# Kernel optimization log

Measured on AMD Instinct MI355X. Metric: run time of the kernel, lower is better.

Reference implementation:

```python
import jax, jax.numpy as jnp
import numpy as np

N_NODES = 100000
N_EDGES = 1280000
D_IN = 64
D_HID = 128
D_OUT = 64


def sage_conv(x, src, dst, W_l, b_l, W_r, n_nodes):
    # PyG SAGEConv (aggr='mean', root_weight=True):
    #   out_i = W_l @ mean_{j in N(i)} x_j + b_l + W_r @ x_i
    msg = x[src]  # [E, d] gather of source-node features
    agg = jax.ops.segment_sum(msg, dst, num_segments=n_nodes)  # [N, d]
    cnt = jax.ops.segment_sum(jnp.ones((src.shape[0], 1), x.dtype), dst,
                              num_segments=n_nodes)  # [N, 1]
    mean = agg / jnp.maximum(cnt, 1.0)  # zero-neighbor nodes -> 0 (matches scatter-mean)
    return mean @ W_l.T + b_l + x @ W_r.T


def setup_inputs() -> dict:
    key = jax.random.key(0)
    ks = jax.random.split(key, 8)
    x = jax.random.normal(ks[0], (N_NODES, D_IN), dtype=jnp.float32)
    edge_index = jax.random.randint(ks[1], (2, N_EDGES), 0, N_NODES, dtype=jnp.int64)
    s = 0.05
    W_l1 = jax.random.normal(ks[2], (D_HID, D_IN), dtype=jnp.float32) * s
    b_l1 = jnp.zeros((D_HID,), dtype=jnp.float32)
    W_r1 = jax.random.normal(ks[3], (D_HID, D_IN), dtype=jnp.float32) * s
    W_l2 = jax.random.normal(ks[4], (D_OUT, D_HID), dtype=jnp.float32) * s
    b_l2 = jnp.zeros((D_OUT,), dtype=jnp.float32)
    W_r2 = jax.random.normal(ks[5], (D_OUT, D_HID), dtype=jnp.float32) * s
    return {"x": x, "edge_index": edge_index,
            "W_l1": W_l1, "b_l1": b_l1, "W_r1": W_r1,
            "W_l2": W_l2, "b_l2": b_l2, "W_r2": W_r2}


def reference(x, edge_index, W_l1, b_l1, W_r1, W_l2, b_l2, W_r2):
    src, dst = edge_index[0], edge_index[1]
    n = x.shape[0]
    h = sage_conv(x, src, dst, W_l1, b_l1, W_r1, n)
    h = jax.nn.relu(h)
    out = sage_conv(h, src, dst, W_l2, b_l2, W_r2, n)
    return out
```

## Files before the change

### kernel.cpp

```cpp
#include <hip/hip_runtime.h>
#include <cstdint>
#include <cstddef>

typedef __attribute__((ext_vector_type(8))) short short8;
typedef __attribute__((ext_vector_type(4))) float floatx4;
typedef __attribute__((ext_vector_type(2))) float floatx2;
typedef __attribute__((ext_vector_type(4))) int intx4;

static constexpr int DIN  = 64;
static constexpr int DHID = 128;
static constexpr int BSH  = 7;
static constexpr int BNODES = 1 << BSH;
static constexpr int TILE = 8192;
static constexpr int CAP  = 4096;
static constexpr unsigned SENT = 0xFFFFFFFFu;

__device__ inline short f2bf(float f) {
  unsigned u = __float_as_uint(f);
  u += 0x7FFF + ((u >> 16) & 1);
  return (short)(u >> 16);
}
__device__ inline float bf2f(short s) {
  return __uint_as_float(((unsigned)(unsigned short)s) << 16);
}
__device__ inline floatx2 bfpair(unsigned u) {
  floatx2 r;
  r[0] = __uint_as_float(u << 16);
  r[1] = __uint_as_float(u & 0xFFFF0000u);
  return r;
}

__global__ __launch_bounds__(256) void part_prep_kernel(const void* edges, long long nmax,
    int* __restrict__ bucket_cursor, int* __restrict__ real_cnt,
    unsigned* __restrict__ packed, int E, int NB,
    const float* __restrict__ x,
    const float* __restrict__ Wl1, const float* __restrict__ Wr1,
    const float* __restrict__ Wl2, const float* __restrict__ Wr2,
    short* __restrict__ xb, short* __restrict__ wc1, short* __restrict__ wc2,
    int nx, int gP, int gx)
{
  __shared__ unsigned sval[TILE];
  __shared__ unsigned saux[TILE];
  __shared__ int hist[1024];
  __shared__ int gb[1024];
  __shared__ int smode;
  int t = threadIdx.x;
  int blk = blockIdx.x;
  if (blk >= gP) {
    int b = blk - gP;
    if (b < gx) {
      int i0 = (b * 256 + t) * 8;
      if (i0 < nx) {
        floatx4 f0 = *(const floatx4*)&x[i0];
        floatx4 f1 = *(const floatx4*)&x[i0 + 4];
        short8 o;
        o[0]=f2bf(f0[0]); o[1]=f2bf(f0[1]); o[2]=f2bf(f0[2]); o[3]=f2bf(f0[3]);
        o[4]=f2bf(f1[0]); o[5]=f2bf(f1[1]); o[6]=f2bf(f1[2]); o[7]=f2bf(f1[3]);
        *(short8*)&xb[i0] = o;
      }
    } else {
      int wb = b - gx;
      int idx = ((wb & 15) * 256 + t) * 4;
      int n = idx >> 7, k = idx & 127;
      const float* src;
      if (wb < 16) src = (k < 64) ? &Wl1[n * 64 + k] : &Wr1[n * 64 + (k - 64)];
      else         src = (n < 64) ? &Wl2[n * 128 + k] : &Wr2[(n - 64) * 128 + k];
      floatx4 f = *(const floatx4*)src;
      short* dst = (wb < 16 ? wc1 : wc2) + idx;
      dst[0]=f2bf(f[0]); dst[1]=f2bf(f[1]); dst[2]=f2bf(f[2]); dst[3]=f2bf(f[3]);
    }
    return;
  }
  int base = blk * TILE;
  int cnt_here = E - base; if (cnt_here > TILE) cnt_here = TILE;
  for (int i = t; i < NB; i += 256) hist[i] = 0;
  if (t == 0) smode = 1;
  __syncthreads();
  {
    const long long* e64 = (const long long*)edges;
    int nchk = E < 256 ? E : 256;
    bool ok = true;
    for (int i = t; i < nchk; i += 256) {
      long long v = e64[i];
      if (v < 0 || v >= nmax) ok = false;
    }
    if (!ok) smode = 0;
  }
  __syncthreads();
  bool m64 = (smode != 0);
  #pragma unroll 4
  for (int c = 0; c < TILE / 256; ++c) {
    int idx = c * 256 + t;
    if (idx < cnt_here) {
      int i = base + idx;
      int s, d;
      if (m64) { const long long* e = (const long long*)edges; s = (int)e[i]; d = (int)e[(size_t)E + i]; }
      else     { const int*       e = (const int*)edges;       s = e[i];      d = e[(size_t)E + i]; }
      int b = d >> BSH;
      int rank = atomicAdd(&hist[b], 1);
      sval[idx] = ((unsigned)(d & (BNODES - 1)) << 17) | (unsigned)s;
      saux[idx] = ((unsigned)b << 13) | (unsigned)rank;
    }
  }
  __syncthreads();
  for (int b = t; b < NB; b += 256) {
    int cnt = hist[b];
    int gbase = 0;
    if (cnt > 0) {
      int pad = (cnt + 15) & ~15;
      gbase = b * CAP + atomicAdd(&bucket_cursor[b], pad);
      atomicAdd(&real_cnt[b], cnt);
      for (int j = cnt; j < pad; ++j) packed[gbase + j] = SENT;
    }
    gb[b] = gbase;
  }
  __syncthreads();
  #pragma unroll 4
  for (int c = 0; c < TILE / 256; ++c) {
    int idx = c * 256 + t;
    if (idx < cnt_here) {
      unsigned a = saux[idx];
      packed[gb[a >> 13] + (a & 0x1FFFu)] = sval[idx];
    }
  }
}

__global__ __launch_bounds__(256) void bucket_sort_kernel(const unsigned* __restrict__ packed,
                                                          const int* __restrict__ bucket_cursor,
                                                          const int* __restrict__ real_cnt,
                                                          int* __restrict__ row_ptr,
                                                          int* __restrict__ sorted_src, int N, int E) {
  __shared__ int nhist[BNODES];
  __shared__ int cur[BNODES];
  __shared__ int wsum[4];
  __shared__ int redsum[4];
  int b = blockIdx.x, t = threadIdx.x;
  int partial = 0;
  for (int i = t; i < b; i += 256) partial += real_cnt[i];
  #pragma unroll
  for (int off = 1; off < 64; off <<= 1) partial += __shfl_xor(partial, off, 64);
  if ((t & 63) == 0) redsum[t >> 6] = partial;
  if (t < BNODES) nhist[t] = 0;
  if (b == 0 && t == 0) row_ptr[N] = E;
  __syncthreads();
  int eb = redsum[0] + redsum[1] + redsum[2] + redsum[3];
  int n0 = b << BSH;
  int nn = N - n0; if (nn > BNODES) nn = BNODES;
  int rbeg = b * CAP, rcnt = bucket_cursor[b];
  for (int i = t; i < rcnt; i += 256) {
    unsigned p = packed[rbeg + i];
    if (p != SENT) atomicAdd(&nhist[p >> 17], 1);
  }
  __syncthreads();
  int lane = t & 63, w = t >> 6;
  int v = (t < BNODES) ? nhist[t] : 0;
  int val = v;
  #pragma unroll
  for (int off = 1; off < 64; off <<= 1) {
    int u = __shfl_up(val, off, 64);
    if (lane >= off) val += u;
  }
  if (lane == 63) wsum[w] = val;
  __syncthreads();
  int pre = (w == 1) ? wsum[0] : 0;
  int excl = pre + val - v;
  if (t < nn) { row_ptr[n0 + t] = eb + excl; cur[t] = eb + excl; }
  __syncthreads();
  for (int i = t; i < rcnt; i += 256) {
    unsigned p = packed[rbeg + i];
    if (p != SENT) {
      int pos = atomicAdd(&cur[p >> 17], 1);
      sorted_src[pos] = (int)(p & 0x1FFFFu);
    }
  }
}

template <bool EPI>
__global__ __launch_bounds__(256) void agg_bf16_kernel(const short* __restrict__ feat,
                                                       const int* __restrict__ row_ptr,
                                                       const int* __restrict__ srcs,
                                                       const float* __restrict__ rbuf,
                                                       const float* __restrict__ bias,
                                                       short* __restrict__ outb,
                                                       float* __restrict__ outf, int N) {
  int node = blockIdx.x * 32 + (threadIdx.x >> 3);
  if (node >= N) return;
  int c = threadIdx.x & 7;
  const short* fbase = feat + c * 8;
  int beg = row_ptr[node], end = row_ptr[node + 1];
  floatx2 acc2[4];
  #pragma unroll
  for (int k = 0; k < 4; ++k) acc2[k] = (floatx2){0.f, 0.f};
  int e = beg;
  for (; e + 8 <= end; e += 8) {
    intx4 sa = *(const intx4*)&srcs[e];
    intx4 sb = *(const intx4*)&srcs[e + 4];
    short8 v0 = *(const short8*)&fbase[(size_t)sa[0] * 64];
    short8 v1 = *(const short8*)&fbase[(size_t)sa[1] * 64];
    short8 v2 = *(const short8*)&fbase[(size_t)sa[2] * 64];
    short8 v3 = *(const short8*)&fbase[(size_t)sa[3] * 64];
    short8 v4 = *(const short8*)&fbase[(size_t)sb[0] * 64];
    short8 v5 = *(const short8*)&fbase[(size_t)sb[1] * 64];
    short8 v6 = *(const short8*)&fbase[(size_t)sb[2] * 64];
    short8 v7 = *(const short8*)&fbase[(size_t)sb[3] * 64];
    const unsigned* u0 = (const unsigned*)&v0;
    const unsigned* u1 = (const unsigned*)&v1;
    const unsigned* u2 = (const unsigned*)&v2;
    const unsigned* u3 = (const unsigned*)&v3;
    const unsigned* u4 = (const unsigned*)&v4;
    const unsigned* u5 = (const unsigned*)&v5;
    const unsigned* u6 = (const unsigned*)&v6;
    const unsigned* u7 = (const unsigned*)&v7;
    #pragma unroll
    for (int k = 0; k < 4; ++k) {
      floatx2 s01 = bfpair(u0[k]) + bfpair(u1[k]);
      floatx2 s23 = bfpair(u2[k]) + bfpair(u3[k]);
      floatx2 s45 = bfpair(u4[k]) + bfpair(u5[k]);
      floatx2 s67 = bfpair(u6[k]) + bfpair(u7[k]);
      acc2[k] += (s01 + s23) + (s45 + s67);
    }
  }
  for (; e + 4 <= end; e += 4) {
    intx4 sa = *(const intx4*)&srcs[e];
    short8 v0 = *(const short8*)&fbase[(size_t)sa[0] * 64];
    short8 v1 = *(const short8*)&fbase[(size_t)sa[1] * 64];
    short8 v2 = *(const short8*)&fbase[(size_t)sa[2] * 64];
    short8 v3 = *(const short8*)&fbase[(size_t)sa[3] * 64];
    const unsigned* u0 = (const unsigned*)&v0;
    const unsigned* u1 = (const unsigned*)&v1;
    const unsigned* u2 = (const unsigned*)&v2;
    const unsigned* u3 = (const unsigned*)&v3;
    #pragma unroll
    for (int k = 0; k < 4; ++k) {
      floatx2 s01 = bfpair(u0[k]) + bfpair(u1[k]);
      floatx2 s23 = bfpair(u2[k]) + bfpair(u3[k]);
      acc2[k] += s01 + s23;
    }
  }
  for (; e < end; ++e) {
    short8 v = *(const short8*)&fbase[(size_t)srcs[e] * 64];
    const unsigned* u = (const unsigned*)&v;
    #pragma unroll
    for (int k = 0; k < 4; ++k) acc2[k] += bfpair(u[k]);
  }
  float acc[8];
  #pragma unroll
  for (int k = 0; k < 4; ++k) { acc[2 * k] = acc2[k][0]; acc[2 * k + 1] = acc2[k][1]; }
  float inv = 1.f / fmaxf((float)(end - beg), 1.f);
  if (!EPI) {
    short8 o;
    #pragma unroll
    for (int j = 0; j < 8; ++j) o[j] = f2bf(acc[j] * inv);
    *(short8*)&outb[(size_t)node * 64 + c * 8] = o;
  } else {
    floatx4 b0 = *(const floatx4*)&bias[c * 8];
    floatx4 b1 = *(const floatx4*)&bias[c * 8 + 4];
    floatx4 r0 = *(const floatx4*)&rbuf[(size_t)node * 64 + c * 8];
    floatx4 r1 = *(const floatx4*)&rbuf[(size_t)node * 64 + c * 8 + 4];
    floatx4 o0, o1;
    #pragma unroll
    for (int j = 0; j < 4; ++j) {
      o0[j] = acc[j] * inv + b0[j] + r0[j];
      o1[j] = acc[4 + j] * inv + b1[j] + r1[j];
    }
    *(floatx4*)&outf[(size_t)node * 64 + c * 8]     = o0;
    *(floatx4*)&outf[(size_t)node * 64 + c * 8 + 4] = o1;
  }
}

__global__ __launch_bounds__(256) void fused_gemm_kernel(
    const short* __restrict__ Aa, const short* __restrict__ Ab,
    const short* __restrict__ wc1, const short* __restrict__ wc2,
    const float* __restrict__ bias1,
    short* __restrict__ Cg, float* __restrict__ Cr, int M)
{
  __shared__ short Ws[128][136];
  __shared__ short Hs[64][136];
  int t = threadIdx.x;
  #pragma unroll
  for (int i = 0; i < 8; ++i) {
    int idx = i * 256 + t;
    int r = idx >> 4, c8 = (idx & 15) * 8;
    *(short8*)&Ws[r][c8] = *(const short8*)&wc1[r * 128 + c8];
  }
  __syncthreads();
  int wv = t >> 6, lane = t & 63, q = lane >> 4, l15 = lane & 15;
  int m0 = blockIdx.x * 64 + wv * 16;
  int row = m0 + l15;
  bool rowok = row < M;
  floatx4 acc[8];
  #pragma unroll
  for (int nt = 0; nt < 8; ++nt) acc[nt] = (floatx4){0.f, 0.f, 0.f, 0.f};
  #pragma unroll
  for (int ko = 0; ko < 4; ++ko) {
    const short* Asrc = (ko < 2) ? Aa : Ab;
    short8 a = {0, 0, 0, 0, 0, 0, 0, 0};
    if (rowok) a = *(const short8*)&Asrc[(size_t)row * 64 + (ko & 1) * 32 + q * 8];
    #pragma unroll
    for (int nt = 0; nt < 8; ++nt) {
      short8 b = *(const short8*)&Ws[nt * 16 + l15][ko * 32 + q * 8];
      acc[nt] = __builtin_amdgcn_mfma_f32_16x16x32_bf16(a, b, acc[nt], 0, 0, 0);
    }
  }
  #pragma unroll
  for (int nt = 0; nt < 8; ++nt) {
    int n = nt * 16 + l15;
    float bv = bias1[n];
    #pragma unroll
    for (int r2 = 0; r2 < 4; ++r2) {
      int lr = wv * 16 + q * 4 + r2;
      float v = fmaxf(acc[nt][r2] + bv, 0.f);
      Hs[lr][n] = f2bf(v);
    }
  }
  __syncthreads();
  #pragma unroll
  for (int i = 0; i < 8; ++i) {
    int idx = i * 256 + t;
    int r = idx >> 4, c8 = (idx & 15) * 8;
    *(short8*)&Ws[r][c8] = *(const short8*)&wc2[r * 128 + c8];
  }
  __syncthreads();
  #pragma unroll
  for (int nt = 0; nt < 8; ++nt) acc[nt] = (floatx4){0.f, 0.f, 0.f, 0.f};
  #pragma unroll
  for (int ko = 0; ko < 4; ++ko) {
    short8 a = *(const short8*)&Hs[wv * 16 + l15][ko * 32 + q * 8];
    #pragma unroll
    for (int nt = 0; nt < 8; ++nt) {
      short8 b = *(const short8*)&Ws[nt * 16 + l15][ko * 32 + q * 8];
      acc[nt] = __builtin_amdgcn_mfma_f32_16x16x32_bf16(a, b, acc[nt], 0, 0, 0);
    }
  }
  #pragma unroll
  for (int nt = 0; nt < 8; ++nt) {
    int n = nt * 16 + l15;
    #pragma unroll
    for (int r2 = 0; r2 < 4; ++r2) {
      int mr = m0 + q * 4 + r2;
      if (mr >= M) continue;
      float v = acc[nt][r2];
      if (nt < 4) Cg[(size_t)mr * 64 + n] = f2bf(v);
      else        Cr[(size_t)mr * 64 + (n - 64)] = v;
    }
  }
}

extern "C" void kernel_launch(void* const* d_in, const int* in_sizes, int n_in,
                              void* d_out, int out_size, void* d_ws, size_t ws_size,
                              hipStream_t stream) {
  const float* x   = (const float*)d_in[0];
  const void*  ei  = d_in[1];
  const float* Wl1 = (const float*)d_in[2];
  const float* bl1 = (const float*)d_in[3];
  const float* Wr1 = (const float*)d_in[4];
  const float* Wl2 = (const float*)d_in[5];
  const float* bl2 = (const float*)d_in[6];
  const float* Wr2 = (const float*)d_in[7];
  int N = in_sizes[0] / DIN;
  int E = in_sizes[1] / 2;
  int NB = (N + BNODES - 1) / BNODES;

  char* w = (char*)d_ws;
  size_t off = 0;
  auto alloc = [&](size_t bytes) -> void* {
    void* p = w + off;
    off += (bytes + 255) & ~(size_t)255;
    return p;
  };
  int*      bcur       = (int*)alloc((size_t)NB * 8);
  int*      rcnt       = bcur + NB;
  int*      row_ptr    = (int*)alloc(((size_t)N + 1) * 4);
  unsigned* packed     = (unsigned*)alloc((size_t)NB * CAP * 4);
  int*      sorted_src = (int*)alloc((size_t)E * 4);
  short*    xb         = (short*)alloc((size_t)N * 64 * 2);
  short*    meanb      = (short*)alloc((size_t)N * 64 * 2);
  float*    rbuf       = (float*)alloc((size_t)N * 64 * 4);
  short*    wc1        = (short*)alloc(128 * 128 * 2);
  short*    wc2        = (short*)alloc(128 * 128 * 2);
  (void)ws_size; (void)n_in; (void)out_size;

  hipMemsetAsync(bcur, 0, (size_t)NB * 8, stream);

  int nx = N * DIN;
  int gx = (nx / 8 + 255) / 256;
  int gP = (E + TILE - 1) / TILE;
  part_prep_kernel<<<gP + gx + 32, 256, 0, stream>>>(ei, (long long)N, bcur, rcnt, packed,
                                                     E, NB, x, Wl1, Wr1, Wl2, Wr2,
                                                     xb, wc1, wc2, nx, gP, gx);

  bucket_sort_kernel<<<NB, 256, 0, stream>>>(packed, bcur, rcnt, row_ptr, sorted_src, N, E);

  int gN32 = (N + 31) / 32;
  agg_bf16_kernel<false><<<gN32, 256, 0, stream>>>(xb, row_ptr, sorted_src, nullptr, nullptr, meanb, nullptr, N);

  int gm = (N + 63) / 64;
  fused_gemm_kernel<<<gm, 256, 0, stream>>>(meanb, xb, wc1, wc2, bl1, meanb, rbuf, N);

  agg_bf16_kernel<true><<<gN32, 256, 0, stream>>>(meanb, row_ptr, sorted_src, rbuf, bl2, nullptr, (float*)d_out, N);
}
```

Before: 203.5 us.

## Fuse first-layer mean aggregation into bucket sort and double GEMM row tile

The bucket sort kernel now keeps each bucket's sorted edge list in shared memory and computes the first-layer neighbor mean for its 128 nodes right away. This removes one kernel launch and the global re-read of row_ptr and sorted_src for the first aggregation. The fused GEMM now handles 128 rows per block, with two MFMA row tiles per wave sharing each B fragment, so fewer weight tiles are loaded into shared memory. In exchange, the sort kernel uses more LDS (a 16KB edge list) and only 128 nodes per block do the gather, which may reduce occupancy and parallelism during aggregation.

After: 201.1 us. No clear change (-1.2%).

```diff
diff --git a/kernel.cpp b/kernel.cpp
--- a/kernel.cpp
+++ b/kernel.cpp
@@ -125,13 +125,14 @@
   }
 }
 
-__global__ __launch_bounds__(256) void bucket_sort_kernel(const unsigned* __restrict__ packed,
-                                                          const int* __restrict__ bucket_cursor,
-                                                          const int* __restrict__ real_cnt,
-                                                          int* __restrict__ row_ptr,
-                                                          int* __restrict__ sorted_src, int N, int E) {
+__global__ __launch_bounds__(256) void bucket_sort_agg_kernel(const unsigned* __restrict__ packed,
+    const int* __restrict__ bucket_cursor, const int* __restrict__ real_cnt,
+    int* __restrict__ row_ptr, int* __restrict__ sorted_src,
+    const short* __restrict__ feat, short* __restrict__ meanb, int N, int E) {
   __shared__ int nhist[BNODES];
   __shared__ int cur[BNODES];
+  __shared__ int begs[BNODES];
+  __shared__ int elist[CAP];
   __shared__ int wsum[4];
   __shared__ int redsum[4];
   int b = blockIdx.x, t = threadIdx.x;
@@ -164,25 +165,81 @@
   __syncthreads();
   int pre = (w == 1) ? wsum[0] : 0;
   int excl = pre + val - v;
-  if (t < nn) { row_ptr[n0 + t] = eb + excl; cur[t] = eb + excl; }
+  if (t < nn) { row_ptr[n0 + t] = eb + excl; cur[t] = excl; begs[t] = excl; }
   __syncthreads();
   for (int i = t; i < rcnt; i += 256) {
     unsigned p = packed[rbeg + i];
     if (p != SENT) {
       int pos = atomicAdd(&cur[p >> 17], 1);
-      sorted_src[pos] = (int)(p & 0x1FFFFu);
-    }
-  }
-}
-
-template <bool EPI>
-__global__ __launch_bounds__(256) void agg_bf16_kernel(const short* __restrict__ feat,
-                                                       const int* __restrict__ row_ptr,
-                                                       const int* __restrict__ srcs,
-                                                       const float* __restrict__ rbuf,
-                                                       const float* __restrict__ bias,
-                                                       short* __restrict__ outb,
-                                                       float* __restrict__ outf, int N) {
+      int s = (int)(p & 0x1FFFFu);
+      elist[pos] = s;
+      sorted_src[eb + pos] = s;
+    }
+  }
+  __syncthreads();
+  int c = t & 7;
+  const short* fbase = feat + c * 8;
+  #pragma unroll
+  for (int ch = 0; ch < 4; ++ch) {
+    int ln = ch * 32 + (t >> 3);
+    if (ln < nn) {
+      int beg = begs[ln], end = cur[ln];
+      floatx2 acc2[4];
+      #pragma unroll
+      for (int k = 0; k < 4; ++k) acc2[k] = (floatx2){0.f, 0.f};
+      int e = beg;
+      for (; e + 8 <= end; e += 8) {
+        int s0 = elist[e],     s1 = elist[e + 1], s2 = elist[e + 2], s3 = elist[e + 3];
+        int s4 = elist[e + 4], s5 = elist[e + 5], s6 = elist[e + 6], s7 = elist[e + 7];
+        short8 v0 = *(const short8*)&fbase[(size_t)s0 * 64];
+        short8 v1 = *(const short8*)&fbase[(size_t)s1 * 64];
+        short8 v2 = *(const short8*)&fbase[(size_t)s2 * 64];
+        short8 v3 = *(const short8*)&fbase[(size_t)s3 * 64];
+        short8 v4 = *(const short8*)&fbase[(size_t)s4 * 64];
+        short8 v5 = *(const short8*)&fbase[(size_t)s5 * 64];
+        short8 v6 = *(const short8*)&fbase[(size_t)s6 * 64];
+        short8 v7 = *(const short8*)&fbase[(size_t)s7 * 64];
+        const unsigned* u0 = (const unsigned*)&v0;
+        const unsigned* u1 = (const unsigned*)&v1;
+        const unsigned* u2 = (const unsigned*)&v2;
+        const unsigned* u3 = (const unsigned*)&v3;
+        const unsigned* u4 = (const unsigned*)&v4;
+        const unsigned* u5 = (const unsigned*)&v5;
+        const unsigned* u6 = (const unsigned*)&v6;
+        const unsigned* u7 = (const unsigned*)&v7;
+        #pragma unroll
+        for (int k = 0; k < 4; ++k) {
+          floatx2 s01 = bfpair(u0[k]) + bfpair(u1[k]);
+          floatx2 s23 = bfpair(u2[k]) + bfpair(u3[k]);
+          floatx2 s45 = bfpair(u4[k]) + bfpair(u5[k]);
+          floatx2 s67 = bfpair(u6[k]) + bfpair(u7[k]);
+          acc2[k] += (s01 + s23) + (s45 + s67);
+        }
+      }
+      for (; e < end; ++e) {
+        short8 vv = *(const short8*)&fbase[(size_t)elist[e] * 64];
+        const unsigned* uu = (const unsigned*)&vv;
+        #pragma unroll
+        for (int k = 0; k < 4; ++k) acc2[k] += bfpair(uu[k]);
+      }
+      float inv = 1.f / fmaxf((float)(end - beg), 1.f);
+      short8 o;
+      #pragma unroll
+      for (int k = 0; k < 4; ++k) {
+        o[2 * k]     = f2bf(acc2[k][0] * inv);
+        o[2 * k + 1] = f2bf(acc2[k][1] * inv);
+      }
+      *(short8*)&meanb[(size_t)(n0 + ln) * 64 + c * 8] = o;
+    }
+  }
+}
+
+__global__ __launch_bounds__(256) void agg_epi_kernel(const short* __restrict__ feat,
+                                                      const int* __restrict__ row_ptr,
+                                                      const int* __restrict__ srcs,
+                                                      const float* __restrict__ rbuf,
+                                                      const float* __restrict__ bias,
+                                                      float* __restrict__ outf, int N) {
   int node = blockIdx.x * 32 + (threadIdx.x >> 3);
   if (node >= N) return;
   int c = threadIdx.x & 7;
@@ -247,25 +304,18 @@
   #pragma unroll
   for (int k = 0; k < 4; ++k) { acc[2 * k] = acc2[k][0]; acc[2 * k + 1] = acc2[k][1]; }
   float inv = 1.f / fmaxf((float)(end - beg), 1.f);
-  if (!EPI) {
-    short8 o;
-    #pragma unroll
-    for (int j = 0; j < 8; ++j) o[j] = f2bf(acc[j] * inv);
-    *(short8*)&outb[(size_t)node * 64 + c * 8] = o;
-  } else {
-    floatx4 b0 = *(const floatx4*)&bias[c * 8];
-    floatx4 b1 = *(const floatx4*)&bias[c * 8 + 4];
-    floatx4 r0 = *(const floatx4*)&rbuf[(size_t)node * 64 + c * 8];
-    floatx4 r1 = *(const floatx4*)&rbuf[(size_t)node * 64 + c * 8 + 4];
-    floatx4 o0, o1;
-    #pragma unroll
-    for (int j = 0; j < 4; ++j) {
-      o0[j] = acc[j] * inv + b0[j] + r0[j];
-      o1[j] = acc[4 + j] * inv + b1[j] + r1[j];
-    }
-    *(floatx4*)&outf[(size_t)node * 64 + c * 8]     = o0;
-    *(floatx4*)&outf[(size_t)node * 64 + c * 8 + 4] = o1;
-  }
+  floatx4 b0 = *(const floatx4*)&bias[c * 8];
+  floatx4 b1 = *(const floatx4*)&bias[c * 8 + 4];
+  floatx4 r0 = *(const floatx4*)&rbuf[(size_t)node * 64 + c * 8];
+  floatx4 r1 = *(const floatx4*)&rbuf[(size_t)node * 64 + c * 8 + 4];
+  floatx4 o0, o1;
+  #pragma unroll
+  for (int j = 0; j < 4; ++j) {
+    o0[j] = acc[j] * inv + b0[j] + r0[j];
+    o1[j] = acc[4 + j] * inv + b1[j] + r1[j];
+  }
+  *(floatx4*)&outf[(size_t)node * 64 + c * 8]     = o0;
+  *(floatx4*)&outf[(size_t)node * 64 + c * 8 + 4] = o1;
 }
 
 __global__ __launch_bounds__(256) void fused_gemm_kernel(
@@ -275,7 +325,7 @@
     short* __restrict__ Cg, float* __restrict__ Cr, int M)
 {
   __shared__ short Ws[128][136];
-  __shared__ short Hs[64][136];
+  __shared__ short Hs[128][136];
   int t = threadIdx.x;
   #pragma unroll
   for (int i = 0; i < 8; ++i) {
@@ -285,32 +335,41 @@
   }
   __syncthreads();
   int wv = t >> 6, lane = t & 63, q = lane >> 4, l15 = lane & 15;
-  int m0 = blockIdx.x * 64 + wv * 16;
-  int row = m0 + l15;
-  bool rowok = row < M;
-  floatx4 acc[8];
-  #pragma unroll
-  for (int nt = 0; nt < 8; ++nt) acc[nt] = (floatx4){0.f, 0.f, 0.f, 0.f};
+  int m0 = blockIdx.x * 128 + wv * 32;
+  floatx4 acc[2][8];
+  #pragma unroll
+  for (int mt = 0; mt < 2; ++mt)
+    #pragma unroll
+    for (int nt = 0; nt < 8; ++nt) acc[mt][nt] = (floatx4){0.f, 0.f, 0.f, 0.f};
   #pragma unroll
   for (int ko = 0; ko < 4; ++ko) {
     const short* Asrc = (ko < 2) ? Aa : Ab;
-    short8 a = {0, 0, 0, 0, 0, 0, 0, 0};
-    if (rowok) a = *(const short8*)&Asrc[(size_t)row * 64 + (ko & 1) * 32 + q * 8];
+    short8 a[2];
+    #pragma unroll
+    for (int mt = 0; mt < 2; ++mt) {
+      int row = m0 + mt * 16 + l15;
+      a[mt] = (short8){0, 0, 0, 0, 0, 0, 0, 0};
+      if (row < M) a[mt] = *(const short8*)&Asrc[(size_t)row * 64 + (ko & 1) * 32 + q * 8];
+    }
     #pragma unroll
     for (int nt = 0; nt < 8; ++nt) {
-      short8 b = *(const short8*)&Ws[nt * 16 + l15][ko * 32 + q * 8];
-      acc[nt] = __builtin_amdgcn_mfma_f32_16x16x32_bf16(a, b, acc[nt], 0, 0, 0);
-    }
-  }
-  #pragma unroll
-  for (int nt = 0; nt < 8; ++nt) {
-    int n = nt * 16 + l15;
-    float bv = bias1[n];
-    #pragma unroll
-    for (int r2 = 0; r2 < 4; ++r2) {
-      int lr = wv * 16 + q * 4 + r2;
-      float v = fmaxf(acc[nt][r2] + bv, 0.f);
-      Hs[lr][n] = f2bf(v);
+      short8 bfr = *(const short8*)&Ws[nt * 16 + l15][ko * 32 + q * 8];
+      acc[0][nt] = __builtin_amdgcn_mfma_f32_16x16x32_bf16(a[0], bfr, acc[0][nt], 0, 0, 0);
+      acc[1][nt] = __builtin_amdgcn_mfma_f32_16x16x32_bf16(a[1], bfr, acc[1][nt], 0, 0, 0);
+    }
+  }
+  #pragma unroll
+  for (int mt = 0; mt < 2; ++mt) {
+    #pragma unroll
+    for (int nt = 0; nt < 8; ++nt) {
+      int n = nt * 16 + l15;
+      float bv = bias1[n];
+      #pragma unroll
+      for (int r2 = 0; r2 < 4; ++r2) {
+        int lr = wv * 32 + mt * 16 + q * 4 + r2;
+        float v = fmaxf(acc[mt][nt][r2] + bv, 0.f);
+        Hs[lr][n] = f2bf(v);
+      }
     }
   }
   __syncthreads();
@@ -322,26 +381,35 @@
   }
   __syncthreads();
   #pragma unroll
-  for (int nt = 0; nt < 8; ++nt) acc[nt] = (floatx4){0.f, 0.f, 0.f, 0.f};
+  for (int mt = 0; mt < 2; ++mt)
+    #pragma unroll
+    for (int nt = 0; nt < 8; ++nt) acc[mt][nt] = (floatx4){0.f, 0.f, 0.f, 0.f};
   #pragma unroll
   for (int ko = 0; ko < 4; ++ko) {
-    short8 a = *(const short8*)&Hs[wv * 16 + l15][ko * 32 + q * 8];
+    short8 a[2];
+    #pragma unroll
+    for (int mt = 0; mt < 2; ++mt)
+      a[mt] = *(const short8*)&Hs[wv * 32 + mt * 16 + l15][ko * 32 + q * 8];
     #pragma unroll
     for (int nt = 0; nt < 8; ++nt) {
-      short8 b = *(const short8*)&Ws[nt * 16 + l15][ko * 32 + q * 8];
-      acc[nt] = __builtin_amdgcn_mfma_f32_16x16x32_bf16(a, b, acc[nt], 0, 0, 0);
-    }
-  }
-  #pragma unroll
-  for (int nt = 0; nt < 8; ++nt) {
-    int n = nt * 16 + l15;
-    #pragma unroll
-    for (int r2 = 0; r2 < 4; ++r2) {
-      int mr = m0 + q * 4 + r2;
-      if (mr >= M) continue;
-      float v = acc[nt][r2];
-      if (nt < 4) Cg[(size_t)mr * 64 + n] = f2bf(v);
-      else        Cr[(size_t)mr * 64 + (n - 64)] = v;
+      short8 bfr = *(const short8*)&Ws[nt * 16 + l15][ko * 32 + q * 8];
+      acc[0][nt] = __builtin_amdgcn_mfma_f32_16x16x32_bf16(a[0], bfr, acc[0][nt], 0, 0, 0);
+      acc[1][nt] = __builtin_amdgcn_mfma_f32_16x16x32_bf16(a[1], bfr, acc[1][nt], 0, 0, 0);
+    }
+  }
+  #pragma unroll
+  for (int mt = 0; mt < 2; ++mt) {
+    #pragma unroll
+    for (int nt = 0; nt < 8; ++nt) {
+      int n = nt * 16 + l15;
+      #pragma unroll
+      for (int r2 = 0; r2 < 4; ++r2) {
+        int mr = m0 + mt * 16 + q * 4 + r2;
+        if (mr >= M) continue;
+        float v = acc[mt][nt][r2];
+        if (nt < 4) Cg[(size_t)mr * 64 + n] = f2bf(v);
+        else        Cr[(size_t)mr * 64 + (n - 64)] = v;
+      }
     }
   }
 }
@@ -389,13 +457,12 @@
                                                      E, NB, x, Wl1, Wr1, Wl2, Wr2,
                                                      xb, wc1, wc2, nx, gP, gx);
 
-  bucket_sort_kernel<<<NB, 256, 0, stream>>>(packed, bcur, rcnt, row_ptr, sorted_src, N, E);
+  bucket_sort_agg_kernel<<<NB, 256, 0, stream>>>(packed, bcur, rcnt, row_ptr, sorted_src,
+                                                 xb, meanb, N, E);
+
+  int gm = (N + 127) / 128;
+  fused_gemm_kernel<<<gm, 256, 0, stream>>>(meanb, xb, wc1, wc2, bl1, meanb, rbuf, N);
 
   int gN32 = (N + 31) / 32;
-  agg_bf16_kernel<false><<<gN32, 256, 0, stream>>>(xb, row_ptr, sorted_src, nullptr, nullptr, meanb, nullptr, N);
-
-  int gm = (N + 63) / 64;
-  fused_gemm_kernel<<<gm, 256, 0, stream>>>(meanb, xb, wc1, wc2, bl1, meanb, rbuf, N);
-
-  agg_bf16_kernel<true><<<gN32, 256, 0, stream>>>(meanb, row_ptr, sorted_src, rbuf, bl2, nullptr, (float*)d_out, N);
-}
+  agg_epi_kernel<<<gN32, 256, 0, stream>>>(meanb, row_ptr, sorted_src, rbuf, bl2, (float*)d_out, N);
+}
```
